# Kernel tuning notes

Hardware: AMD Instinct MI355X
Metric: run time of the kernel (lower is better)

Reference implementation:

```python
import jax, jax.numpy as jnp
import numpy as np

B, H, W, C, NH, WS = 64, 56, 56, 128, 4, 7
N = H * W


def setup_inputs() -> dict:
    key = jax.random.key(0)
    ks = jax.random.split(key, 6)
    return {
        "x": jax.random.normal(ks[0], (B, N, C), jnp.float32),
        "w_qkv": jax.random.normal(ks[1], (3 * C, C), jnp.float32) * 0.02,
        "w_lim": jax.random.normal(ks[2], (C, 1, 3, 3), jnp.float32) * 0.02,
        "b_lim": jax.random.normal(ks[3], (C,), jnp.float32) * 0.02,
        "w_proj": jax.random.normal(ks[4], (C, C), jnp.float32) * 0.02,
        "b_proj": jax.random.normal(ks[5], (C,), jnp.float32) * 0.02,
        "H": H,
        "W": W,
    }


def reference(x, w_qkv, w_lim, b_lim, w_proj, b_proj, H, W):
    Bq, Nq, Cq = x.shape
    ws, nh = WS, NH
    hd = Cq // nh
    hg, wg = H // ws, W // ws  # 8, 8 -- no padding needed at these shapes
    scale = hd ** -0.5

    qkv = x @ w_qkv.T                      # (B, N, 3C)
    q, k, v = jnp.split(qkv, 3, axis=-1)

    def img2win(t):
        # (B,N,C) -> (B, hg*wg, nh, ws*ws, hd)
        t = t.reshape(Bq, hg, ws, wg, ws, Cq).transpose(0, 1, 3, 2, 4, 5)
        return t.reshape(Bq, hg * wg, ws * ws, nh, hd).transpose(0, 1, 3, 2, 4)

    qw, kw, vw = img2win(q), img2win(k), img2win(v)

    # LIM: depthwise 3x3 conv on shape-integrated V (win2img(img2win(v)) == v as NCHW)
    v_img = v.reshape(Bq, H, W, Cq).transpose(0, 3, 1, 2)     # (B,C,H,W)
    v_lim = jax.lax.conv_general_dilated(
        v_img, w_lim, window_strides=(1, 1), padding='SAME',
        dimension_numbers=('NCHW', 'OIHW', 'NCHW'), feature_group_count=Cq)
    v_lim = v_lim + b_lim[None, :, None, None]
    v_lim = v_lim.reshape(Bq, Cq, Nq).transpose(0, 2, 1)      # (B,N,C)

    # windowed attention: g = window index, n = head
    attn = jax.nn.softmax(
        jnp.einsum('bgnqd,bgnkd->bgnqk', qw, kw) * scale, axis=-1)
    out = jnp.einsum('bgnqk,bgnkd->bgnqd', attn, vw)          # (B,g,nh,ws*ws,hd)

    # merge windows back: (B,g,nh,ws*ws,hd) -> (B,N,C)
    out = out.transpose(0, 1, 3, 2, 4).reshape(Bq, hg, wg, ws, ws, Cq)
    out = out.transpose(0, 1, 3, 2, 4, 5).reshape(Bq, Nq, Cq)

    out = out + v_lim
    return out @ w_proj.T + b_proj
```

## Files before the change

kernel.cpp:

```cpp
#include <hip/hip_runtime.h>
#include <cstdint>

#define B_   64
#define H_   56
#define W_   56
#define C_   128
#define WSZ  7
#define TT   49
#define NN   3136
#define MM   (B_ * NN)
#define SCALE 0.17677669529663687f

typedef short bf16x8 __attribute__((ext_vector_type(8)));
typedef short bf16x4 __attribute__((ext_vector_type(4)));
typedef float f32x4  __attribute__((ext_vector_type(4)));
typedef unsigned short u16;

__device__ __forceinline__ float bf2f(u16 u) {
    return __uint_as_float(((unsigned int)u) << 16);
}
__device__ __forceinline__ u16 f2bf(float f) {
    unsigned int u = __float_as_uint(f);
    u += 0x7FFFu + ((u >> 16) & 1u);
    return (u16)(u >> 16);
}

__global__ __launch_bounds__(256) void kw_cvt(
    const float* __restrict__ wqkv, const float* __restrict__ wproj,
    u16* __restrict__ wqbf, u16* __restrict__ wpbf)
{
    int g = blockIdx.x * 256 + threadIdx.x;
    if (g < 12288) {
        float4 f = *(const float4*)&wqkv[g * 4];
        float mul = (g < 4096) ? SCALE : 1.0f;
        ushort4 u;
        u.x = f2bf(f.x * mul); u.y = f2bf(f.y * mul);
        u.z = f2bf(f.z * mul); u.w = f2bf(f.w * mul);
        *(ushort4*)&wqbf[g * 4] = u;
    } else {
        int g2 = g - 12288;
        float4 f = *(const float4*)&wproj[g2 * 4];
        ushort4 u;
        u.x = f2bf(f.x); u.y = f2bf(f.y);
        u.z = f2bf(f.z); u.w = f2bf(f.w);
        *(ushort4*)&wpbf[g2 * 4] = u;
    }
}

template <bool PREW>
__global__ __launch_bounds__(256, 3) void ka_fused(
    const float* __restrict__ x, const float* __restrict__ wqkv,
    const u16* __restrict__ wqbf,
    u16* __restrict__ vout, float* __restrict__ out)
{
    __shared__ u16 lds[26240];
    u16 (*xq)[136] = (u16(*)[136])&lds[0];
    u16 (*ks)[136] = (u16(*)[136])&lds[8704];
    u16 (*vs)[138] = (u16(*)[138])&lds[17408];
    u16* ps_ = &lds[0];

    const int t   = threadIdx.x;
    const int blk = blockIdx.x;
    const int b_  = blk >> 6, wr = blk & 63;
    const int qy  = wr >> 3, qx = wr & 7;
    const int wave = t >> 6, lane = t & 63, lr = lane & 15, quad = lane >> 4;

    for (int i = t; i < 64 * 32; i += 256) {
        int tok = i >> 5, c4 = (i & 31) * 4;
        ushort4 u4 = {0, 0, 0, 0};
        if (tok < TT) {
            int hh = qy * WSZ + tok / WSZ, ww = qx * WSZ + tok % WSZ;
            float4 f = *(const float4*)&x[((size_t)b_ * NN + hh * W_ + ww) * C_ + c4];
            u4.x = f2bf(f.x); u4.y = f2bf(f.y);
            u4.z = f2bf(f.z); u4.w = f2bf(f.w);
        }
        *(ushort4*)&xq[tok][c4] = u4;
    }
    __syncthreads();

#pragma unroll
    for (int cc = 0; cc < 2; cc++) {
        const int ch = 1 + cc;
        u16* dstbase = cc ? &vs[0][0] : &ks[0][0];
        const int dstride = cc ? 138 : 136;
#pragma unroll
        for (int half = 0; half < 2; half++) {
            const int wrowi = ch * 128 + half * 64 + wave * 16 + lr;
            const float* wrowf = &wqkv[(size_t)wrowi * C_];
            const u16*   wrowb = &wqbf[(size_t)wrowi * C_];
            f32x4 acc[4];
#pragma unroll
            for (int mi = 0; mi < 4; mi++) acc[mi] = {0.f, 0.f, 0.f, 0.f};
#pragma unroll
            for (int kk = 0; kk < 4; kk++) {
                bf16x8 bfr;
                if constexpr (PREW) {
                    bfr = *(const bf16x8*)&wrowb[kk * 32 + quad * 8];
                } else {
                    float4 f0 = *(const float4*)&wrowf[kk * 32 + quad * 8];
                    float4 f1 = *(const float4*)&wrowf[kk * 32 + quad * 8 + 4];
                    bfr[0] = (short)f2bf(f0.x); bfr[1] = (short)f2bf(f0.y);
                    bfr[2] = (short)f2bf(f0.z); bfr[3] = (short)f2bf(f0.w);
                    bfr[4] = (short)f2bf(f1.x); bfr[5] = (short)f2bf(f1.y);
                    bfr[6] = (short)f2bf(f1.z); bfr[7] = (short)f2bf(f1.w);
                }
#pragma unroll
                for (int mi = 0; mi < 4; mi++) {
                    bf16x8 afr = *(const bf16x8*)&xq[mi * 16 + lr][kk * 32 + quad * 8];
                    acc[mi] = __builtin_amdgcn_mfma_f32_16x16x32_bf16(
                        afr, bfr, acc[mi], 0, 0, 0);
                }
            }
#pragma unroll
            for (int mi = 0; mi < 4; mi++) {
#pragma unroll
                for (int r = 0; r < 4; r++) {
                    int tok = mi * 16 + quad * 4 + r;
                    int col = half * 64 + wave * 16 + lr;
                    u16 bv = f2bf(acc[mi][r]);
                    dstbase[tok * dstride + col] = bv;
                    if (cc == 1 && tok < TT) {
                        int hh2 = qy * WSZ + tok / WSZ;
                        int ww2 = qx * WSZ + tok % WSZ;
                        vout[((size_t)b_ * NN + hh2 * W_ + ww2) * C_ + col] = bv;
                    }
                }
            }
        }
    }

    const float qmul = PREW ? 1.0f : SCALE;
    f32x4 qacc[2][4];
#pragma unroll
    for (int half = 0; half < 2; half++)
#pragma unroll
        for (int mi = 0; mi < 4; mi++) qacc[half][mi] = {0.f, 0.f, 0.f, 0.f};
#pragma unroll
    for (int half = 0; half < 2; half++) {
        const int wrowi = half * 64 + wave * 16 + lr;
        const float* wrowf = &wqkv[(size_t)wrowi * C_];
        const u16*   wrowb = &wqbf[(size_t)wrowi * C_];
#pragma unroll
        for (int kk = 0; kk < 4; kk++) {
            bf16x8 bfr;
            if constexpr (PREW) {
                bfr = *(const bf16x8*)&wrowb[kk * 32 + quad * 8];
            } else {
                float4 f0 = *(const float4*)&wrowf[kk * 32 + quad * 8];
                float4 f1 = *(const float4*)&wrowf[kk * 32 + quad * 8 + 4];
                bfr[0] = (short)f2bf(f0.x); bfr[1] = (short)f2bf(f0.y);
                bfr[2] = (short)f2bf(f0.z); bfr[3] = (short)f2bf(f0.w);
                bfr[4] = (short)f2bf(f1.x); bfr[5] = (short)f2bf(f1.y);
                bfr[6] = (short)f2bf(f1.z); bfr[7] = (short)f2bf(f1.w);
            }
#pragma unroll
            for (int mi = 0; mi < 4; mi++) {
                bf16x8 afr = *(const bf16x8*)&xq[mi * 16 + lr][kk * 32 + quad * 8];
                qacc[half][mi] = __builtin_amdgcn_mfma_f32_16x16x32_bf16(
                    afr, bfr, qacc[half][mi], 0, 0, 0);
            }
        }
    }
    __syncthreads();

#pragma unroll
    for (int half = 0; half < 2; half++)
#pragma unroll
        for (int mi = 0; mi < 4; mi++)
#pragma unroll
            for (int r = 0; r < 4; r++)
                xq[mi * 16 + quad * 4 + r][half * 64 + wave * 16 + lr] =
                    f2bf(qacc[half][mi][r] * qmul);
    __syncthreads();

    const int h = wave;
    bf16x8 qf[4], kf[4];
#pragma unroll
    for (int mi = 0; mi < 4; mi++) {
        qf[mi] = *(const bf16x8*)&xq[mi * 16 + lr][h * 32 + quad * 8];
        kf[mi] = *(const bf16x8*)&ks[mi * 16 + lr][h * 32 + quad * 8];
    }
    __syncthreads();

    f32x4 s[4][4];
#pragma unroll
    for (int mi = 0; mi < 4; mi++)
#pragma unroll
        for (int nj = 0; nj < 4; nj++) s[mi][nj] = {0.f, 0.f, 0.f, 0.f};
#pragma unroll
    for (int mi = 0; mi < 4; mi++)
#pragma unroll
        for (int nj = 0; nj < 4; nj++)
            s[mi][nj] = __builtin_amdgcn_mfma_f32_16x16x32_bf16(
                qf[mi], kf[nj], s[mi][nj], 0, 0, 0);

    if (lr >= 1) {
#pragma unroll
        for (int mi = 0; mi < 4; mi++)
#pragma unroll
            for (int r = 0; r < 4; r++) s[mi][3][r] = -1e30f;
    }

    float rsum[4][4];
#pragma unroll
    for (int mi = 0; mi < 4; mi++) {
#pragma unroll
        for (int r = 0; r < 4; r++) {
            float mx = fmaxf(fmaxf(s[mi][0][r], s[mi][1][r]),
                             fmaxf(s[mi][2][r], s[mi][3][r]));
#pragma unroll
            for (int off = 1; off < 16; off <<= 1)
                mx = fmaxf(mx, __shfl_xor(mx, off));
            float sum = 0.f;
#pragma unroll
            for (int nj = 0; nj < 4; nj++) {
                float p = __expf(s[mi][nj][r] - mx);
                s[mi][nj][r] = p;
                sum += p;
            }
#pragma unroll
            for (int off = 1; off < 16; off <<= 1)
                sum += __shfl_xor(sum, off);
            rsum[mi][r] = sum;
        }
    }

#pragma unroll
    for (int mi = 0; mi < 4; mi++)
#pragma unroll
        for (int nj = 0; nj < 4; nj++)
#pragma unroll
            for (int r = 0; r < 4; r++)
                ps_[((h * 64) + mi * 16 + quad * 4 + r) * 68 + nj * 16 + lr] =
                    f2bf(s[mi][nj][r]);

    f32x4 o[4][2];
#pragma unroll
    for (int mi = 0; mi < 4; mi++)
#pragma unroll
        for (int nv = 0; nv < 2; nv++) o[mi][nv] = {0.f, 0.f, 0.f, 0.f};

#pragma unroll
    for (int kt = 0; kt < 2; kt++) {
        bf16x8 pf[4];
#pragma unroll
        for (int mi = 0; mi < 4; mi++) {
            const u16* pp = &ps_[((h * 64) + mi * 16 + lr) * 68 + kt * 32 + quad * 8];
            bf16x4 lo = *(const bf16x4*)&pp[0];
            bf16x4 hi = *(const bf16x4*)&pp[4];
            bf16x8 f;
            f[0] = lo[0]; f[1] = lo[1]; f[2] = lo[2]; f[3] = lo[3];
            f[4] = hi[0]; f[5] = hi[1]; f[6] = hi[2]; f[7] = hi[3];
            pf[mi] = f;
        }
        bf16x8 vf[2];
#pragma unroll
        for (int nv = 0; nv < 2; nv++) {
            bf16x8 tmp;
#pragma unroll
            for (int jj = 0; jj < 8; jj++)
                tmp[jj] = (short)vs[kt * 32 + quad * 8 + jj][h * 32 + nv * 16 + lr];
            vf[nv] = tmp;
        }
#pragma unroll
        for (int mi = 0; mi < 4; mi++)
#pragma unroll
            for (int nv = 0; nv < 2; nv++)
                o[mi][nv] = __builtin_amdgcn_mfma_f32_16x16x32_bf16(
                    pf[mi], vf[nv], o[mi][nv], 0, 0, 0);
    }

#pragma unroll
    for (int mi = 0; mi < 4; mi++) {
#pragma unroll
        for (int r = 0; r < 4; r++) {
            int i = mi * 16 + quad * 4 + r;
            if (i < TT) {
                int hh = qy * WSZ + i / WSZ, ww = qx * WSZ + i % WSZ;
                size_t orow = (size_t)b_ * NN + hh * W_ + ww;
                float inv = 1.f / rsum[mi][r];
#pragma unroll
                for (int nv = 0; nv < 2; nv++)
                    out[orow * C_ + h * 32 + nv * 16 + lr] = o[mi][nv][r] * inv;
            }
        }
    }
}

__global__ __launch_bounds__(256) void kb_lim(
    const u16* __restrict__ v, const float* __restrict__ wlim,
    const float* __restrict__ blim, float* __restrict__ out)
{
    const int t   = threadIdx.x;
    const int pos = blockIdx.x * 16 + (t >> 4);
    const int c0  = (t & 15) * 8;
    const int b_  = pos / NN;
    const int rem = pos - b_ * NN;
    const int hh  = rem / W_;
    const int ww  = rem - hh * W_;

    float w72[72];
    {
        const float* wp = &wlim[c0 * 9];
#pragma unroll
        for (int i = 0; i < 18; i++) {
            float4 f = *(const float4*)&wp[i * 4];
            w72[i * 4 + 0] = f.x; w72[i * 4 + 1] = f.y;
            w72[i * 4 + 2] = f.z; w72[i * 4 + 3] = f.w;
        }
    }
    float acc[8];
    {
        float4 b0 = *(const float4*)&blim[c0];
        float4 b1 = *(const float4*)&blim[c0 + 4];
        acc[0] = b0.x; acc[1] = b0.y; acc[2] = b0.z; acc[3] = b0.w;
        acc[4] = b1.x; acc[5] = b1.y; acc[6] = b1.z; acc[7] = b1.w;
    }

    const u16* vbase = &v[(size_t)b_ * NN * C_ + c0];
#pragma unroll
    for (int dy = -1; dy <= 1; dy++) {
        int y = hh + dy;
        bool yok = (unsigned)y < (unsigned)H_;
#pragma unroll
        for (int dx = -1; dx <= 1; dx++) {
            int x2 = ww + dx;
            bool ok = yok && ((unsigned)x2 < (unsigned)W_);
            bf16x8 vv = {0, 0, 0, 0, 0, 0, 0, 0};
            if (ok) vv = *(const bf16x8*)&vbase[(size_t)(y * W_ + x2) * C_];
            const int tap = (dy + 1) * 3 + (dx + 1);
#pragma unroll
            for (int j = 0; j < 8; j++)
                acc[j] += bf2f((u16)vv[j]) * w72[j * 9 + tap];
        }
    }

    float* op = &out[(size_t)pos * C_ + c0];
    float4 o0 = *(const float4*)&op[0];
    float4 o1 = *(const float4*)&op[4];
    o0.x += acc[0]; o0.y += acc[1]; o0.z += acc[2]; o0.w += acc[3];
    o1.x += acc[4]; o1.y += acc[5]; o1.z += acc[6]; o1.w += acc[7];
    *(float4*)&op[0] = o0;
    *(float4*)&op[4] = o1;
}

template <bool PREW>
__global__ __launch_bounds__(256) void kc_proj(
    float* __restrict__ y, const float* __restrict__ wproj,
    const u16* __restrict__ wpbf, const float* __restrict__ bproj)
{
    __shared__ u16 As[128][72];
    __shared__ u16 Ws[128][72];
    const int t    = threadIdx.x;
    const int m0   = blockIdx.x * 128;
    const int wave = t >> 6, lane = t & 63, lr = lane & 15, quad = lane >> 4;
    const int wm = (wave >> 1) * 64, wn = (wave & 1) * 64;

    f32x4 acc[4][4];
#pragma unroll
    for (int mi = 0; mi < 4; mi++)
#pragma unroll
        for (int ni = 0; ni < 4; ni++) acc[mi][ni] = {0.f, 0.f, 0.f, 0.f};

#pragma unroll
    for (int kt = 0; kt < 2; kt++) {
        const int k0 = kt * 64;
#pragma unroll
        for (int p = 0; p < 8; p++) {
            int e   = p * 256 + t;
            int row = e >> 4;
            int col = (e & 15) * 4;
            float4 fa = *(const float4*)&y[(size_t)(m0 + row) * C_ + k0 + col];
            ushort4 ua;
            ua.x = f2bf(fa.x); ua.y = f2bf(fa.y);
            ua.z = f2bf(fa.z); ua.w = f2bf(fa.w);
            *(ushort4*)&As[row][col] = ua;
            if constexpr (!PREW) {
                float4 fw = *(const float4*)&wproj[(size_t)row * C_ + k0 + col];
                ushort4 uw;
                uw.x = f2bf(fw.x); uw.y = f2bf(fw.y);
                uw.z = f2bf(fw.z); uw.w = f2bf(fw.w);
                *(ushort4*)&Ws[row][col] = uw;
            }
        }
        if constexpr (PREW) {
#pragma unroll
            for (int p4 = 0; p4 < 4; p4++) {
                int e    = p4 * 256 + t;
                int row  = e >> 3;
                int col8 = (e & 7) * 8;
                *(bf16x8*)&Ws[row][col8] =
                    *(const bf16x8*)&wpbf[(size_t)row * C_ + k0 + col8];
            }
        }
        __syncthreads();
#pragma unroll
        for (int kk = 0; kk < 2; kk++) {
            bf16x8 a[4], b[4];
#pragma unroll
            for (int mi = 0; mi < 4; mi++)
                a[mi] = *(const bf16x8*)&As[wm + mi * 16 + lr][kk * 32 + quad * 8];
#pragma unroll
            for (int ni = 0; ni < 4; ni++)
                b[ni] = *(const bf16x8*)&Ws[wn + ni * 16 + lr][kk * 32 + quad * 8];
#pragma unroll
            for (int mi = 0; mi < 4; mi++)
#pragma unroll
                for (int ni = 0; ni < 4; ni++)
                    acc[mi][ni] = __builtin_amdgcn_mfma_f32_16x16x32_bf16(
                        a[mi], b[ni], acc[mi][ni], 0, 0, 0);
        }
        if (kt == 0) __syncthreads();
    }

#pragma unroll
    for (int mi = 0; mi < 4; mi++) {
#pragma unroll
        for (int r = 0; r < 4; r++) {
            int m = m0 + wm + mi * 16 + quad * 4 + r;
#pragma unroll
            for (int ni = 0; ni < 4; ni++) {
                int c = wn + ni * 16 + lr;
                y[(size_t)m * C_ + c] = acc[mi][ni][r] + bproj[c];
            }
        }
    }
}

extern "C" void kernel_launch(void* const* d_in, const int* in_sizes, int n_in,
                              void* d_out, int out_size, void* d_ws, size_t ws_size,
                              hipStream_t stream)
{
    const float* x     = (const float*)d_in[0];
    const float* wqkv  = (const float*)d_in[1];
    const float* wlim  = (const float*)d_in[2];
    const float* blim  = (const float*)d_in[3];
    const float* wproj = (const float*)d_in[4];
    const float* bproj = (const float*)d_in[5];
    float* out = (float*)d_out;
    u16*   v   = (u16*)d_ws;

    const size_t vbytes = (size_t)MM * C_ * 2;
    const size_t need   = vbytes + (49152 + 16384) * 2;

    if (ws_size >= need) {
        u16* wqbf = (u16*)((char*)d_ws + vbytes);
        u16* wpbf = wqbf + 49152;
        kw_cvt<<<dim3(64), 256, 0, stream>>>(wqkv, wproj, wqbf, wpbf);
        ka_fused<true><<<dim3(B_ * 64), 256, 0, stream>>>(x, wqkv, wqbf, v, out);
        kb_lim  <<<dim3(MM / 16), 256, 0, stream>>>(v, wlim, blim, out);
        kc_proj<true><<<dim3(MM / 128), 256, 0, stream>>>(out, wproj, wpbf, bproj);
    } else {
        ka_fused<false><<<dim3(B_ * 64), 256, 0, stream>>>(x, wqkv, nullptr, v, out);
        kb_lim  <<<dim3(MM / 16), 256, 0, stream>>>(v, wlim, blim, out);
        kc_proj<false><<<dim3(MM / 128), 256, 0, stream>>>(out, wproj, nullptr, bproj);
    }
}
```

Before: 386.1 us.

## Fuse depthwise LIM conv into projection GEMM A-tile load

Removes the separate LIM kernel and computes the 3x3 depthwise conv plus bias on the fly while staging the projection GEMM's A tile into shared memory. This avoids a full read-modify-write pass over the fp32 intermediate output. In exchange, each thread performs nine neighbor loads of v per row with narrower 4-element loads, and register pressure rises inside the GEMM prologue.

```diff
diff --git a/kernel.cpp b/kernel.cpp
--- a/kernel.cpp
+++ b/kernel.cpp
@@ -287,67 +287,12 @@
     }
 }
 
-__global__ __launch_bounds__(256) void kb_lim(
-    const u16* __restrict__ v, const float* __restrict__ wlim,
-    const float* __restrict__ blim, float* __restrict__ out)
-{
-    const int t   = threadIdx.x;
-    const int pos = blockIdx.x * 16 + (t >> 4);
-    const int c0  = (t & 15) * 8;
-    const int b_  = pos / NN;
-    const int rem = pos - b_ * NN;
-    const int hh  = rem / W_;
-    const int ww  = rem - hh * W_;
-
-    float w72[72];
-    {
-        const float* wp = &wlim[c0 * 9];
-#pragma unroll
-        for (int i = 0; i < 18; i++) {
-            float4 f = *(const float4*)&wp[i * 4];
-            w72[i * 4 + 0] = f.x; w72[i * 4 + 1] = f.y;
-            w72[i * 4 + 2] = f.z; w72[i * 4 + 3] = f.w;
-        }
-    }
-    float acc[8];
-    {
-        float4 b0 = *(const float4*)&blim[c0];
-        float4 b1 = *(const float4*)&blim[c0 + 4];
-        acc[0] = b0.x; acc[1] = b0.y; acc[2] = b0.z; acc[3] = b0.w;
-        acc[4] = b1.x; acc[5] = b1.y; acc[6] = b1.z; acc[7] = b1.w;
-    }
-
-    const u16* vbase = &v[(size_t)b_ * NN * C_ + c0];
-#pragma unroll
-    for (int dy = -1; dy <= 1; dy++) {
-        int y = hh + dy;
-        bool yok = (unsigned)y < (unsigned)H_;
-#pragma unroll
-        for (int dx = -1; dx <= 1; dx++) {
-            int x2 = ww + dx;
-            bool ok = yok && ((unsigned)x2 < (unsigned)W_);
-            bf16x8 vv = {0, 0, 0, 0, 0, 0, 0, 0};
-            if (ok) vv = *(const bf16x8*)&vbase[(size_t)(y * W_ + x2) * C_];
-            const int tap = (dy + 1) * 3 + (dx + 1);
-#pragma unroll
-            for (int j = 0; j < 8; j++)
-                acc[j] += bf2f((u16)vv[j]) * w72[j * 9 + tap];
-        }
-    }
-
-    float* op = &out[(size_t)pos * C_ + c0];
-    float4 o0 = *(const float4*)&op[0];
-    float4 o1 = *(const float4*)&op[4];
-    o0.x += acc[0]; o0.y += acc[1]; o0.z += acc[2]; o0.w += acc[3];
-    o1.x += acc[4]; o1.y += acc[5]; o1.z += acc[6]; o1.w += acc[7];
-    *(float4*)&op[0] = o0;
-    *(float4*)&op[4] = o1;
-}
-
 template <bool PREW>
 __global__ __launch_bounds__(256) void kc_proj(
-    float* __restrict__ y, const float* __restrict__ wproj,
-    const u16* __restrict__ wpbf, const float* __restrict__ bproj)
+    float* __restrict__ y, const u16* __restrict__ v,
+    const float* __restrict__ wlim, const float* __restrict__ blim,
+    const float* __restrict__ wproj, const u16* __restrict__ wpbf,
+    const float* __restrict__ bproj)
 {
     __shared__ u16 As[128][72];
     __shared__ u16 Ws[128][72];
@@ -355,6 +300,7 @@
     const int m0   = blockIdx.x * 128;
     const int wave = t >> 6, lane = t & 63, lr = lane & 15, quad = lane >> 4;
     const int wm = (wave >> 1) * 64, wn = (wave & 1) * 64;
+    const int colc = (t & 15) * 4;
 
     f32x4 acc[4][4];
 #pragma unroll
@@ -365,24 +311,57 @@
 #pragma unroll
     for (int kt = 0; kt < 2; kt++) {
         const int k0 = kt * 64;
+        const int c0 = k0 + colc;
+
+        float wl[36];
+        {
+            const float* wp = &wlim[c0 * 9];
+#pragma unroll
+            for (int i = 0; i < 9; i++) {
+                float4 f = *(const float4*)&wp[i * 4];
+                wl[i * 4 + 0] = f.x; wl[i * 4 + 1] = f.y;
+                wl[i * 4 + 2] = f.z; wl[i * 4 + 3] = f.w;
+            }
+        }
+        float4 bl = *(const float4*)&blim[c0];
+
 #pragma unroll
         for (int p = 0; p < 8; p++) {
-            int e   = p * 256 + t;
-            int row = e >> 4;
-            int col = (e & 15) * 4;
-            float4 fa = *(const float4*)&y[(size_t)(m0 + row) * C_ + k0 + col];
+            int row = p * 16 + (t >> 4);
+            int pos = m0 + row;
+            int b_  = pos / NN;
+            int rem = pos - b_ * NN;
+            int hh  = rem / W_;
+            int ww  = rem - hh * W_;
+
+            float4 fa = *(const float4*)&y[(size_t)pos * C_ + c0];
+            float z0 = fa.x + bl.x, z1 = fa.y + bl.y;
+            float z2 = fa.z + bl.z, z3 = fa.w + bl.w;
+
+            const u16* vb = &v[(size_t)b_ * NN * C_ + c0];
+#pragma unroll
+            for (int dy = -1; dy <= 1; dy++) {
+                int yy = hh + dy;
+                bool yok = (unsigned)yy < (unsigned)H_;
+#pragma unroll
+                for (int dx = -1; dx <= 1; dx++) {
+                    int x2 = ww + dx;
+                    bool ok = yok && ((unsigned)x2 < (unsigned)W_);
+                    bf16x4 vv = {0, 0, 0, 0};
+                    if (ok) vv = *(const bf16x4*)&vb[(size_t)(yy * W_ + x2) * C_];
+                    const int tap = (dy + 1) * 3 + (dx + 1);
+                    z0 += bf2f((u16)vv[0]) * wl[0 * 9 + tap];
+                    z1 += bf2f((u16)vv[1]) * wl[1 * 9 + tap];
+                    z2 += bf2f((u16)vv[2]) * wl[2 * 9 + tap];
+                    z3 += bf2f((u16)vv[3]) * wl[3 * 9 + tap];
+                }
+            }
             ushort4 ua;
-            ua.x = f2bf(fa.x); ua.y = f2bf(fa.y);
-            ua.z = f2bf(fa.z); ua.w = f2bf(fa.w);
-            *(ushort4*)&As[row][col] = ua;
-            if constexpr (!PREW) {
-                float4 fw = *(const float4*)&wproj[(size_t)row * C_ + k0 + col];
-                ushort4 uw;
-                uw.x = f2bf(fw.x); uw.y = f2bf(fw.y);
-                uw.z = f2bf(fw.z); uw.w = f2bf(fw.w);
-                *(ushort4*)&Ws[row][col] = uw;
-            }
-        }
+            ua.x = f2bf(z0); ua.y = f2bf(z1);
+            ua.z = f2bf(z2); ua.w = f2bf(z3);
+            *(ushort4*)&As[row][colc] = ua;
+        }
+
         if constexpr (PREW) {
 #pragma unroll
             for (int p4 = 0; p4 < 4; p4++) {
@@ -391,6 +370,17 @@
                 int col8 = (e & 7) * 8;
                 *(bf16x8*)&Ws[row][col8] =
                     *(const bf16x8*)&wpbf[(size_t)row * C_ + k0 + col8];
+            }
+        } else {
+#pragma unroll
+            for (int p = 0; p < 8; p++) {
+                int e   = p * 256 + t;
+                int row = e >> 4;
+                float4 fw = *(const float4*)&wproj[(size_t)row * C_ + k0 + colc];
+                ushort4 uw;
+                uw.x = f2bf(fw.x); uw.y = f2bf(fw.y);
+                uw.z = f2bf(fw.z); uw.w = f2bf(fw.w);
+                *(ushort4*)&Ws[row][colc] = uw;
             }
         }
         __syncthreads();
@@ -448,11 +438,11 @@
         u16* wpbf = wqbf + 49152;
         kw_cvt<<<dim3(64), 256, 0, stream>>>(wqkv, wproj, wqbf, wpbf);
         ka_fused<true><<<dim3(B_ * 64), 256, 0, stream>>>(x, wqkv, wqbf, v, out);
-        kb_lim  <<<dim3(MM / 16), 256, 0, stream>>>(v, wlim, blim, out);
-        kc_proj<true><<<dim3(MM / 128), 256, 0, stream>>>(out, wproj, wpbf, bproj);
+        kc_proj<true><<<dim3(MM / 128), 256, 0, stream>>>(
+            out, v, wlim, blim, wproj, wpbf, bproj);
     } else {
         ka_fused<false><<<dim3(B_ * 64), 256, 0, stream>>>(x, wqkv, nullptr, v, out);
-        kb_lim  <<<dim3(MM / 16), 256, 0, stream>>>(v, wlim, blim, out);
-        kc_proj<false><<<dim3(MM / 128), 256, 0, stream>>>(out, wproj, nullptr, bproj);
-    }
-}
+        kc_proj<false><<<dim3(MM / 128), 256, 0, stream>>>(
+            out, v, wlim, blim, wproj, nullptr, bproj);
+    }
+}
```

Result: slower. 497.3 us (+28.8%).
